# Kernel tuning notes

Hardware: AMD Instinct MI355X
Metric: run time of the kernel (lower is better)

Reference implementation:

```python
import jax, jax.numpy as jnp
import numpy as np

N_HEADS = 8
D_MODEL = 512
HEAD_DIM = D_MODEL // N_HEADS


def setup_inputs() -> dict:
    key = jax.random.key(0)
    ks = jax.random.split(key, 9)
    B, T1, T2, D = 1, 4096, 4096, D_MODEL
    w_scale = 0.02
    return {
        "query": jax.random.normal(ks[0], (B, T1, D), dtype=jnp.float32),
        "key": jax.random.normal(ks[1], (B, T2, D), dtype=jnp.float32),
        "value": jax.random.normal(ks[2], (B, T2, D), dtype=jnp.float32),
        # True = padded (masked out); ~half positions masked
        "key_padding_mask": jax.random.randint(ks[3], (B, T2), 0, 2) == 1,
        "Wq_w": jax.random.normal(ks[4], (D, D), dtype=jnp.float32) * w_scale,
        "Wq_b": jnp.zeros((D,), dtype=jnp.float32),
        "Wk_w": jax.random.normal(ks[5], (D, D), dtype=jnp.float32) * w_scale,
        "Wk_b": jnp.zeros((D,), dtype=jnp.float32),
        "Wv_w": jax.random.normal(ks[6], (D, D), dtype=jnp.float32) * w_scale,
        "Wv_b": jnp.zeros((D,), dtype=jnp.float32),
        "Wo_w": jax.random.normal(ks[7], (D, D), dtype=jnp.float32) * w_scale,
        "Wo_b": jnp.zeros((D,), dtype=jnp.float32),
    }


def reference(query, key, value, key_padding_mask,
              Wq_w, Wq_b, Wk_w, Wk_b, Wv_w, Wv_b, Wo_w, Wo_b):
    B, T1, D = query.shape
    T2 = key.shape[1]
    H, HD = N_HEADS, HEAD_DIM

    # torch Linear: y = x @ W.T + b
    q = (query @ Wq_w.T + Wq_b).reshape(B, T1, H, HD).transpose(0, 2, 1, 3)  # [B,H,T1,HD]
    k = (key @ Wk_w.T + Wk_b).reshape(B, T2, H, HD).transpose(0, 2, 1, 3)    # [B,H,T2,HD]
    v = (value @ Wv_w.T + Wv_b).reshape(B, T2, H, HD).transpose(0, 2, 1, 3)  # [B,H,T2,HD]

    scale = 1.0 / (HD ** 0.5)
    scores = jnp.einsum("bhqd,bhkd->bhqk", q, k) * scale                     # [B,H,T1,T2]
    mask_value = jnp.finfo(scores.dtype).min
    scores = jnp.where(key_padding_mask[:, None, None, :], mask_value, scores)

    attn = jax.nn.softmax(scores, axis=-1)                                   # [B,H,T1,T2]
    # dropout p=0.0 (inference) -> identity

    out = jnp.einsum("bhqk,bhkd->bhqd", attn, v)                             # [B,H,T1,HD]
    out = out.transpose(0, 2, 1, 3).reshape(B, T1, D)
    out = out @ Wo_w.T + Wo_b
    return (out, attn)
```

## Files before the change

kernel.cpp:

```cpp
#include <hip/hip_runtime.h>
#include <hip/hip_bf16.h>
#include <float.h>
#include <stdint.h>

typedef __bf16 bf16x8 __attribute__((ext_vector_type(8)));
typedef __bf16 bf16x4 __attribute__((ext_vector_type(4)));
typedef float  f32x4  __attribute__((ext_vector_type(4)));

#define T_SEQ 4096
#define DMODEL 512
#define NH 8
#define HDIM 64
#define KS1 4
#define L2E 1.44269504088896340736f

__device__ __forceinline__ float fexp2(float x) { return __builtin_amdgcn_exp2f(x); }

__device__ __forceinline__ void gl_lds16(const __bf16* g, char* l) {
    __builtin_amdgcn_global_load_lds(
        (const __attribute__((address_space(1))) unsigned int*)(g),
        (__attribute__((address_space(3))) unsigned int*)(l),
        16, 0, 0);
}

__global__ __launch_bounds__(256) void qkv_kernel(
    const float* __restrict__ qin, const float* __restrict__ kin, const float* __restrict__ vin,
    const float* __restrict__ Wq, const float* __restrict__ bq,
    const float* __restrict__ Wk, const float* __restrict__ bk,
    const float* __restrict__ Wv, const float* __restrict__ bv,
    __bf16* __restrict__ qo, __bf16* __restrict__ ko, __bf16* __restrict__ vt)
{
    __shared__ char lds[16384];
    char* Ab = lds;
    char* Bb = lds + 8192;

    const int z = blockIdx.z;
    const float* X    = (z == 0) ? qin : (z == 1) ? kin : vin;
    const float* W    = (z == 0) ? Wq  : (z == 1) ? Wk  : Wv;
    const float* bias = (z == 0) ? bq  : (z == 1) ? bk  : bv;

    const int m0 = blockIdx.x * 64;
    const int n0 = blockIdx.y * 64;
    const int tid  = threadIdx.x;
    const int w    = tid >> 6;
    const int lane = tid & 63;
    const int lrow = lane & 15;
    const int lgrp = lane >> 4;

    f32x4 acc[4] = {};
    const int r  = tid >> 2;
    const int c0 = (tid & 3) * 16;

    for (int kt = 0; kt < 8; ++kt) {
        const int k0 = kt * 64;
        const float* gA = X + (size_t)(m0 + r) * DMODEL + k0 + c0;
        const float* gB = W + (size_t)(n0 + r) * DMODEL + k0 + c0;
        const int sw = (r & 7) << 4;
#pragma unroll
        for (int i = 0; i < 4; ++i) {
            float4 a4 = *(const float4*)(gA + 4 * i);
            float4 b4 = *(const float4*)(gB + 4 * i);
            bf16x4 av, bv4;
            av[0] = (__bf16)a4.x; av[1] = (__bf16)a4.y; av[2] = (__bf16)a4.z; av[3] = (__bf16)a4.w;
            bv4[0] = (__bf16)b4.x; bv4[1] = (__bf16)b4.y; bv4[2] = (__bf16)b4.z; bv4[3] = (__bf16)b4.w;
            *(bf16x4*)(Ab + r * 128 + ((c0 * 2 + 8 * i) ^ sw)) = av;
            *(bf16x4*)(Bb + r * 128 + ((c0 * 2 + 8 * i) ^ sw)) = bv4;
        }
        __syncthreads();
#pragma unroll
        for (int ks = 0; ks < 2; ++ks) {
            bf16x8 af = *(const bf16x8*)(Ab + (w * 16 + lrow) * 128 +
                                         ((ks * 64 + lgrp * 16) ^ ((lrow & 7) << 4)));
#pragma unroll
            for (int ns = 0; ns < 4; ++ns) {
                bf16x8 bf = *(const bf16x8*)(Bb + (ns * 16 + lrow) * 128 +
                                             ((ks * 64 + lgrp * 16) ^ ((lrow & 7) << 4)));
                acc[ns] = __builtin_amdgcn_mfma_f32_16x16x32_bf16(af, bf, acc[ns], 0, 0, 0);
            }
        }
        __syncthreads();
    }

    if (z == 2) {
        char* LT = lds;
#pragma unroll
        for (int ns = 0; ns < 4; ++ns) {
            float bcol = bias[n0 + ns * 16 + lrow];
#pragma unroll
            for (int rr = 0; rr < 4; ++rr) {
                int col = ns * 16 + lrow;
                int row = w * 16 + lgrp * 4 + rr;
                *(__bf16*)(LT + col * 128 + ((row * 2) ^ ((col & 7) << 4))) =
                    (__bf16)(acc[ns][rr] + bcol);
            }
        }
        __syncthreads();
        int d  = tid >> 2;
        int nb = (tid & 3) * 32;
        bf16x8 t0 = *(const bf16x8*)(LT + d * 128 + (nb ^ ((d & 7) << 4)));
        bf16x8 t1 = *(const bf16x8*)(LT + d * 128 + ((nb + 16) ^ ((d & 7) << 4)));
        __bf16* dst = vt + (size_t)(n0 + d) * T_SEQ + m0 + (tid & 3) * 16;
        *(bf16x8*)dst = t0;
        *(bf16x8*)(dst + 8) = t1;
    } else {
        __bf16* out = (z == 0) ? qo : ko;
        const float sc = (z == 0) ? 0.125f : 1.0f;
#pragma unroll
        for (int ns = 0; ns < 4; ++ns) {
            float bcol = bias[n0 + ns * 16 + lrow];
#pragma unroll
            for (int rr = 0; rr < 4; ++rr) {
                int orow = m0 + w * 16 + lgrp * 4 + rr;
                out[(size_t)orow * DMODEL + n0 + ns * 16 + lrow] =
                    (__bf16)((acc[ns][rr] + bcol) * sc);
            }
        }
    }
}

__global__ __launch_bounds__(256) void attn_stats(
    const __bf16* __restrict__ qb, const __bf16* __restrict__ kb,
    const int* __restrict__ mask, float* __restrict__ l_part)
{
    __shared__ char lds[16384];
    char* KB0 = lds;
    char* KB1 = lds + 8192;

    const int b    = blockIdx.x;
    const int rmap = (b & 7) * ((64 * NH * KS1) / 8) + (b >> 3);
    const int qbi  = rmap & 63;
    const int h    = (rmap >> 6) & (NH - 1);
    const int ksp  = rmap >> 9;
    const int q0   = qbi * 64;
    const int k0   = ksp * (T_SEQ / KS1);

    const int tid  = threadIdx.x;
    const int w    = tid >> 6;
    const int lane = tid & 63;
    const int lrow = lane & 15;
    const int lgrp = lane >> 4;
    const int swl  = (lrow & 7) << 4;

    bf16x8 qa[2];
    {
        const __bf16* qp = qb + (size_t)(q0 + w * 16 + lrow) * DMODEL + h * HDIM;
        qa[0] = *(const bf16x8*)(qp + lgrp * 8);
        qa[1] = *(const bf16x8*)(qp + 32 + lgrp * 8);
    }

    const int key0 = w * 16 + (lane >> 3);
    const int key1 = key0 + 8;
    const int g    = lane & 7;
    const __bf16* sK0 = kb + (size_t)(k0 + key0) * DMODEL + h * HDIM + (g ^ (key0 & 7)) * 8;
    const __bf16* sK1 = kb + (size_t)(k0 + key1) * DMODEL + h * HDIM + (g ^ (key1 & 7)) * 8;

    float lsum[4] = {0.f, 0.f, 0.f, 0.f};

    gl_lds16(sK0, KB0 + w * 2048);
    gl_lds16(sK1, KB0 + w * 2048 + 1024);
    __syncthreads();

    char* cur = KB0;
    char* nxt = KB1;
    const int NT = (T_SEQ / KS1) / 64;
    for (int kt = 0; kt < NT; ++kt) {
        if (kt + 1 < NT) {
            gl_lds16(sK0 + (size_t)(kt + 1) * 64 * DMODEL, nxt + w * 2048);
            gl_lds16(sK1 + (size_t)(kt + 1) * 64 * DMODEL, nxt + w * 2048 + 1024);
        }
        float bias[4][4];
#pragma unroll
        for (int ns = 0; ns < 4; ++ns) {
            int4 mi = *(const int4*)(mask + k0 + kt * 64 + ns * 16 + lgrp * 4);
            bias[ns][0] = mi.x ? -1e30f : 0.f;
            bias[ns][1] = mi.y ? -1e30f : 0.f;
            bias[ns][2] = mi.z ? -1e30f : 0.f;
            bias[ns][3] = mi.w ? -1e30f : 0.f;
        }

        f32x4 acc[4] = {};
        __builtin_amdgcn_s_setprio(1);
#pragma unroll
        for (int ns = 0; ns < 4; ++ns) {
            bf16x8 kf0 = *(const bf16x8*)(cur + (ns * 16 + lrow) * 128 + ((lgrp * 16) ^ swl));
            bf16x8 kf1 = *(const bf16x8*)(cur + (ns * 16 + lrow) * 128 + ((64 + lgrp * 16) ^ swl));
            acc[ns] = __builtin_amdgcn_mfma_f32_16x16x32_bf16(kf0, qa[0], acc[ns], 0, 0, 0);
            acc[ns] = __builtin_amdgcn_mfma_f32_16x16x32_bf16(kf1, qa[1], acc[ns], 0, 0, 0);
        }
        __builtin_amdgcn_s_setprio(0);
#pragma unroll
        for (int ns = 0; ns < 4; ++ns)
#pragma unroll
            for (int rr = 0; rr < 4; ++rr)
                lsum[ns] += fexp2(fmaf(acc[ns][rr], L2E, bias[ns][rr]));
        __syncthreads();
        char* t = cur; cur = nxt; nxt = t;
    }

    float tot = (lsum[0] + lsum[1]) + (lsum[2] + lsum[3]);
    tot += __shfl_xor(tot, 16);
    tot += __shfl_xor(tot, 32);
    if (lgrp == 0)
        l_part[((size_t)h * KS1 + ksp) * T_SEQ + q0 + w * 16 + lrow] = tot;
}

__global__ __launch_bounds__(256) void attn_main(
    const __bf16* __restrict__ qb, const __bf16* __restrict__ kb,
    const __bf16* __restrict__ vt, const int* __restrict__ mask,
    const float* __restrict__ l_part,
    float* __restrict__ attn_out, void* __restrict__ opart,
    int KSP2, int of32)
{
    __shared__ char lds[40960];
    char* KB0 = lds;
    char* KB1 = lds + 8192;
    char* VB0 = lds + 16384;
    char* VB1 = lds + 24576;
    char* PB  = lds + 32768;

    const int nwg  = 64 * NH * KSP2;
    const int b    = blockIdx.x;
    const int rmap = (b & 7) * (nwg >> 3) + (b >> 3);
    const int qbi  = rmap & 63;
    const int h    = (rmap >> 6) & (NH - 1);
    const int kz   = rmap >> 9;
    const int q0   = qbi * 64;
    const int kspan = T_SEQ / KSP2;
    const int k0   = kz * kspan;
    const int NT   = kspan / 64;

    const int tid  = threadIdx.x;
    const int w    = tid >> 6;
    const int lane = tid & 63;
    const int lrow = lane & 15;
    const int lgrp = lane >> 4;
    const int swl  = (lrow & 7) << 4;

    bf16x8 qa[2];
    {
        const __bf16* qp = qb + (size_t)(q0 + w * 16 + lrow) * DMODEL + h * HDIM;
        qa[0] = *(const bf16x8*)(qp + lgrp * 8);
        qa[1] = *(const bf16x8*)(qp + 32 + lgrp * 8);
    }

    float rl;
    {
        float s = 0.f;
#pragma unroll
        for (int ks = 0; ks < KS1; ++ks)
            s += l_part[((size_t)h * KS1 + ks) * T_SEQ + q0 + w * 16 + lrow];
        rl = 1.0f / s;
    }

    const int key0 = w * 16 + (lane >> 3);
    const int key1 = key0 + 8;
    const int g    = lane & 7;
    const __bf16* sK0 = kb + (size_t)(k0 + key0) * DMODEL + h * HDIM + (g ^ (key0 & 7)) * 8;
    const __bf16* sK1 = kb + (size_t)(k0 + key1) * DMODEL + h * HDIM + (g ^ (key1 & 7)) * 8;
    const __bf16* sV0 = vt + (size_t)(h * HDIM + key0) * T_SEQ + k0 + (g ^ (key0 & 7)) * 8;
    const __bf16* sV1 = vt + (size_t)(h * HDIM + key1) * T_SEQ + k0 + (g ^ (key1 & 7)) * 8;

    f32x4 oacc[4] = {};
    float* arow = attn_out + (size_t)h * T_SEQ * T_SEQ +
                  (size_t)(q0 + w * 16 + lrow) * T_SEQ + k0 + lgrp * 4;
    char* Pw = PB + w * 2048;

    gl_lds16(sK0, KB0 + w * 2048);
    gl_lds16(sK1, KB0 + w * 2048 + 1024);
    gl_lds16(sV0, VB0 + w * 2048);
    gl_lds16(sV1, VB0 + w * 2048 + 1024);
    __syncthreads();

    char *kc = KB0, *kn = KB1, *vc = VB0, *vn = VB1;
    for (int kt = 0; kt < NT; ++kt) {
        if (kt + 1 < NT) {
            gl_lds16(sK0 + (size_t)(kt + 1) * 64 * DMODEL, kn + w * 2048);
            gl_lds16(sK1 + (size_t)(kt + 1) * 64 * DMODEL, kn + w * 2048 + 1024);
            gl_lds16(sV0 + (size_t)(kt + 1) * 64,          vn + w * 2048);
            gl_lds16(sV1 + (size_t)(kt + 1) * 64,          vn + w * 2048 + 1024);
        }
        float bias[4][4];
#pragma unroll
        for (int ns = 0; ns < 4; ++ns) {
            int4 mi = *(const int4*)(mask + k0 + kt * 64 + ns * 16 + lgrp * 4);
            bias[ns][0] = mi.x ? -1e30f : 0.f;
            bias[ns][1] = mi.y ? -1e30f : 0.f;
            bias[ns][2] = mi.z ? -1e30f : 0.f;
            bias[ns][3] = mi.w ? -1e30f : 0.f;
        }

        f32x4 acc[4] = {};
        __builtin_amdgcn_s_setprio(1);
#pragma unroll
        for (int ns = 0; ns < 4; ++ns) {
            bf16x8 kf0 = *(const bf16x8*)(kc + (ns * 16 + lrow) * 128 + ((lgrp * 16) ^ swl));
            bf16x8 kf1 = *(const bf16x8*)(kc + (ns * 16 + lrow) * 128 + ((64 + lgrp * 16) ^ swl));
            acc[ns] = __builtin_amdgcn_mfma_f32_16x16x32_bf16(kf0, qa[0], acc[ns], 0, 0, 0);
            acc[ns] = __builtin_amdgcn_mfma_f32_16x16x32_bf16(kf1, qa[1], acc[ns], 0, 0, 0);
        }
        __builtin_amdgcn_s_setprio(0);

        f32x4 pvs[4];
#pragma unroll
        for (int ns = 0; ns < 4; ++ns) {
            f32x4 pv;
#pragma unroll
            for (int rr = 0; rr < 4; ++rr)
                pv[rr] = fexp2(fmaf(acc[ns][rr], L2E, bias[ns][rr])) * rl;
            pvs[ns] = pv;
            bf16x4 pb;
            pb[0] = (__bf16)pv[0]; pb[1] = (__bf16)pv[1];
            pb[2] = (__bf16)pv[2]; pb[3] = (__bf16)pv[3];
            *(bf16x4*)(Pw + lrow * 128 + ((ns * 32 + lgrp * 8) ^ swl)) = pb;
        }

        __builtin_amdgcn_s_setprio(1);
#pragma unroll
        for (int ks = 0; ks < 2; ++ks) {
            bf16x8 pa = *(const bf16x8*)(Pw + lrow * 128 + ((ks * 64 + lgrp * 16) ^ swl));
#pragma unroll
            for (int dsb = 0; dsb < 4; ++dsb) {
                bf16x8 vf = *(const bf16x8*)(vc + (dsb * 16 + lrow) * 128 +
                                             ((ks * 64 + lgrp * 16) ^ swl));
                oacc[dsb] = __builtin_amdgcn_mfma_f32_16x16x32_bf16(vf, pa, oacc[dsb], 0, 0, 0);
            }
        }
        __builtin_amdgcn_s_setprio(0);

#pragma unroll
        for (int ns = 0; ns < 4; ++ns)
            *(f32x4*)(arow + kt * 64 + ns * 16) = pvs[ns];

        __syncthreads();
        char* t;
        t = kc; kc = kn; kn = t;
        t = vc; vc = vn; vn = t;
    }

    if (of32) {
        float* op = (float*)opart + (size_t)kz * T_SEQ * DMODEL +
                    (size_t)(q0 + w * 16 + lrow) * DMODEL + h * HDIM + lgrp * 4;
#pragma unroll
        for (int dsb = 0; dsb < 4; ++dsb)
            *(f32x4*)(op + dsb * 16) = oacc[dsb];
    } else {
        __bf16* op = (__bf16*)opart + (size_t)(q0 + w * 16 + lrow) * DMODEL + h * HDIM + lgrp * 4;
#pragma unroll
        for (int dsb = 0; dsb < 4; ++dsb) {
            bf16x4 ob;
            ob[0] = (__bf16)oacc[dsb][0]; ob[1] = (__bf16)oacc[dsb][1];
            ob[2] = (__bf16)oacc[dsb][2]; ob[3] = (__bf16)oacc[dsb][3];
            *(bf16x4*)(op + dsb * 16) = ob;
        }
    }
}

__global__ __launch_bounds__(256) void oproj_kernel(
    const void* __restrict__ opart, const float* __restrict__ Wo,
    const float* __restrict__ bo, float* __restrict__ out, int KSP2, int of32)
{
    __shared__ char lds[16384];
    char* Ab = lds;
    char* Bb = lds + 8192;

    const int m0 = blockIdx.x * 64;
    const int n0 = blockIdx.y * 64;
    const int tid  = threadIdx.x;
    const int w    = tid >> 6;
    const int lane = tid & 63;
    const int lrow = lane & 15;
    const int lgrp = lane >> 4;

    f32x4 acc[4] = {};
    const int r   = tid >> 2;
    const int c0e = (tid & 3) * 16;
    const int sw  = (r & 7) << 4;

    for (int kt = 0; kt < 8; ++kt) {
        const int k0 = kt * 64;
        if (of32) {
            const float* p0 = (const float*)opart + (size_t)(m0 + r) * DMODEL + k0 + c0e;
#pragma unroll
            for (int i = 0; i < 4; ++i) {
                f32x4 a4 = *(const f32x4*)(p0 + 4 * i);
                for (int s = 1; s < KSP2; ++s)
                    a4 = a4 + *(const f32x4*)(p0 + (size_t)s * T_SEQ * DMODEL + 4 * i);
                bf16x4 av;
                av[0] = (__bf16)a4[0]; av[1] = (__bf16)a4[1];
                av[2] = (__bf16)a4[2]; av[3] = (__bf16)a4[3];
                *(bf16x4*)(Ab + r * 128 + ((c0e * 2 + 8 * i) ^ sw)) = av;
            }
        } else {
            const __bf16* pa = (const __bf16*)opart + (size_t)(m0 + r) * DMODEL + k0 + c0e;
            bf16x8 a0 = *(const bf16x8*)pa;
            bf16x8 a1 = *(const bf16x8*)(pa + 8);
            *(bf16x8*)(Ab + r * 128 + ((c0e * 2) ^ sw)) = a0;
            *(bf16x8*)(Ab + r * 128 + ((c0e * 2 + 16) ^ sw)) = a1;
        }
        const float* gB = Wo + (size_t)(n0 + r) * DMODEL + k0 + c0e;
#pragma unroll
        for (int i = 0; i < 4; ++i) {
            float4 b4 = *(const float4*)(gB + 4 * i);
            bf16x4 bv4;
            bv4[0] = (__bf16)b4.x; bv4[1] = (__bf16)b4.y;
            bv4[2] = (__bf16)b4.z; bv4[3] = (__bf16)b4.w;
            *(bf16x4*)(Bb + r * 128 + ((c0e * 2 + 8 * i) ^ sw)) = bv4;
        }
        __syncthreads();
#pragma unroll
        for (int ks = 0; ks < 2; ++ks) {
            bf16x8 af = *(const bf16x8*)(Ab + (w * 16 + lrow) * 128 +
                                         ((ks * 64 + lgrp * 16) ^ ((lrow & 7) << 4)));
#pragma unroll
            for (int ns = 0; ns < 4; ++ns) {
                bf16x8 bf = *(const bf16x8*)(Bb + (ns * 16 + lrow) * 128 +
                                             ((ks * 64 + lgrp * 16) ^ ((lrow & 7) << 4)));
                acc[ns] = __builtin_amdgcn_mfma_f32_16x16x32_bf16(af, bf, acc[ns], 0, 0, 0);
            }
        }
        __syncthreads();
    }

#pragma unroll
    for (int ns = 0; ns < 4; ++ns) {
        float bcol = bo[n0 + ns * 16 + lrow];
#pragma unroll
        for (int rr = 0; rr < 4; ++rr) {
            int orow = m0 + w * 16 + lgrp * 4 + rr;
            out[(size_t)orow * DMODEL + n0 + ns * 16 + lrow] = acc[ns][rr] + bcol;
        }
    }
}

extern "C" void kernel_launch(void* const* d_in, const int* in_sizes, int n_in,
                              void* d_out, int out_size, void* d_ws, size_t ws_size,
                              hipStream_t stream) {
    const float* query = (const float*)d_in[0];
    const float* key   = (const float*)d_in[1];
    const float* value = (const float*)d_in[2];
    const int*   mask  = (const int*)d_in[3];
    const float* Wq = (const float*)d_in[4];
    const float* bq = (const float*)d_in[5];
    const float* Wk = (const float*)d_in[6];
    const float* bk = (const float*)d_in[7];
    const float* Wv = (const float*)d_in[8];
    const float* bv = (const float*)d_in[9];
    const float* Wo = (const float*)d_in[10];
    const float* bo = (const float*)d_in[11];

    float* out  = (float*)d_out;
    float* attn = out + (size_t)T_SEQ * DMODEL;

    char* ws = (char*)d_ws;
    __bf16* qo     = (__bf16*)(ws);
    __bf16* ko     = (__bf16*)(ws + (4u << 20));
    __bf16* vt     = (__bf16*)(ws + (8u << 20));
    float*  l_part = (float*)(ws + (12u << 20));
    void*   opart  = (void*)(ws + (12u << 20) + (1u << 19));
    const size_t obase = (12u << 20) + (1u << 19);

    int KSP2, of32;
    const size_t oslice = (size_t)T_SEQ * DMODEL * 4;
    if (ws_size >= obase + 4 * oslice)      { KSP2 = 4; of32 = 1; }
    else if (ws_size >= obase + 2 * oslice) { KSP2 = 2; of32 = 1; }
    else if (ws_size >= obase + oslice)     { KSP2 = 1; of32 = 1; }
    else                                    { KSP2 = 1; of32 = 0; }

    qkv_kernel<<<dim3(64, 8, 3), 256, 0, stream>>>(query, key, value,
                                                   Wq, bq, Wk, bk, Wv, bv, qo, ko, vt);
    attn_stats<<<dim3(64 * NH * KS1), 256, 0, stream>>>(qo, ko, mask, l_part);
    attn_main<<<dim3(64 * NH * KSP2), 256, 0, stream>>>(qo, ko, vt, mask, l_part,
                                                        attn, opart, KSP2, of32);
    oproj_kernel<<<dim3(64, 8), 256, 0, stream>>>(opart, Wo, bo, out, KSP2, of32);
}
```

Before: 256.2 us.

## Triple-buffer K/V tiles with explicit vmcnt waits and stage mask bias in LDS

Replaces the double-buffered K/V LDS pipeline with a three-stage ring, prefetching two tiles ahead and replacing the per-iteration __syncthreads with a partial s_waitcnt vmcnt plus s_barrier, so attention-probability stores need not drain before the next tile. The key-padding mask for the block's key span is converted once into an LDS bias array instead of being re-read from global memory every tile. Attention-probability stores are interleaved with the exp computation rather than batched after the PV MFMAs. LDS use grows to 60 KB per block, which may lower occupancy, and the hand-tuned vmcnt counts depend on the exact number of outstanding global ops.

After: 268.2 us. +4.7%, slower.

```diff
diff --git a/kernel.cpp b/kernel.cpp
--- a/kernel.cpp
+++ b/kernel.cpp
@@ -211,12 +211,9 @@
     float* __restrict__ attn_out, void* __restrict__ opart,
     int KSP2, int of32)
 {
-    __shared__ char lds[40960];
-    char* KB0 = lds;
-    char* KB1 = lds + 8192;
-    char* VB0 = lds + 16384;
-    char* VB1 = lds + 24576;
-    char* PB  = lds + 32768;
+    __shared__ char lds[61440];
+    char* PB = lds + 49152;
+    char* MB = lds + 57344;
 
     const int nwg  = 64 * NH * KSP2;
     const int b    = blockIdx.x;
@@ -252,6 +249,16 @@
         rl = 1.0f / s;
     }
 
+    {
+        int4 mi = *(const int4*)(mask + k0 + tid * 4);
+        f32x4 mb;
+        mb[0] = mi.x ? -1e30f : 0.f;
+        mb[1] = mi.y ? -1e30f : 0.f;
+        mb[2] = mi.z ? -1e30f : 0.f;
+        mb[3] = mi.w ? -1e30f : 0.f;
+        *(f32x4*)(MB + tid * 16) = mb;
+    }
+
     const int key0 = w * 16 + (lane >> 3);
     const int key1 = key0 + 8;
     const int g    = lane & 7;
@@ -260,58 +267,55 @@
     const __bf16* sV0 = vt + (size_t)(h * HDIM + key0) * T_SEQ + k0 + (g ^ (key0 & 7)) * 8;
     const __bf16* sV1 = vt + (size_t)(h * HDIM + key1) * T_SEQ + k0 + (g ^ (key1 & 7)) * 8;
 
+#define STAGE(tt, buf) do {                                             \
+        size_t koff_ = (size_t)(tt) * 64 * DMODEL;                      \
+        size_t voff_ = (size_t)(tt) * 64;                               \
+        gl_lds16(sK0 + koff_, (buf) + w * 2048);                        \
+        gl_lds16(sK1 + koff_, (buf) + w * 2048 + 1024);                 \
+        gl_lds16(sV0 + voff_, (buf) + 8192 + w * 2048);                 \
+        gl_lds16(sV1 + voff_, (buf) + 8192 + w * 2048 + 1024);          \
+    } while (0)
+
     f32x4 oacc[4] = {};
     float* arow = attn_out + (size_t)h * T_SEQ * T_SEQ +
                   (size_t)(q0 + w * 16 + lrow) * T_SEQ + k0 + lgrp * 4;
     char* Pw = PB + w * 2048;
 
-    gl_lds16(sK0, KB0 + w * 2048);
-    gl_lds16(sK1, KB0 + w * 2048 + 1024);
-    gl_lds16(sV0, VB0 + w * 2048);
-    gl_lds16(sV1, VB0 + w * 2048 + 1024);
+    char* bA = lds;
+    char* bB = lds + 16384;
+    char* bC = lds + 32768;
+
+    STAGE(0, bA);
+    STAGE(1, bB);
     __syncthreads();
 
-    char *kc = KB0, *kn = KB1, *vc = VB0, *vn = VB1;
     for (int kt = 0; kt < NT; ++kt) {
-        if (kt + 1 < NT) {
-            gl_lds16(sK0 + (size_t)(kt + 1) * 64 * DMODEL, kn + w * 2048);
-            gl_lds16(sK1 + (size_t)(kt + 1) * 64 * DMODEL, kn + w * 2048 + 1024);
-            gl_lds16(sV0 + (size_t)(kt + 1) * 64,          vn + w * 2048);
-            gl_lds16(sV1 + (size_t)(kt + 1) * 64,          vn + w * 2048 + 1024);
-        }
-        float bias[4][4];
-#pragma unroll
-        for (int ns = 0; ns < 4; ++ns) {
-            int4 mi = *(const int4*)(mask + k0 + kt * 64 + ns * 16 + lgrp * 4);
-            bias[ns][0] = mi.x ? -1e30f : 0.f;
-            bias[ns][1] = mi.y ? -1e30f : 0.f;
-            bias[ns][2] = mi.z ? -1e30f : 0.f;
-            bias[ns][3] = mi.w ? -1e30f : 0.f;
-        }
+        if (kt + 2 < NT) STAGE(kt + 2, bC);
+        __builtin_amdgcn_sched_barrier(0);
 
         f32x4 acc[4] = {};
         __builtin_amdgcn_s_setprio(1);
 #pragma unroll
         for (int ns = 0; ns < 4; ++ns) {
-            bf16x8 kf0 = *(const bf16x8*)(kc + (ns * 16 + lrow) * 128 + ((lgrp * 16) ^ swl));
-            bf16x8 kf1 = *(const bf16x8*)(kc + (ns * 16 + lrow) * 128 + ((64 + lgrp * 16) ^ swl));
+            bf16x8 kf0 = *(const bf16x8*)(bA + (ns * 16 + lrow) * 128 + ((lgrp * 16) ^ swl));
+            bf16x8 kf1 = *(const bf16x8*)(bA + (ns * 16 + lrow) * 128 + ((64 + lgrp * 16) ^ swl));
             acc[ns] = __builtin_amdgcn_mfma_f32_16x16x32_bf16(kf0, qa[0], acc[ns], 0, 0, 0);
             acc[ns] = __builtin_amdgcn_mfma_f32_16x16x32_bf16(kf1, qa[1], acc[ns], 0, 0, 0);
         }
         __builtin_amdgcn_s_setprio(0);
 
-        f32x4 pvs[4];
-#pragma unroll
-        for (int ns = 0; ns < 4; ++ns) {
+#pragma unroll
+        for (int ns = 0; ns < 4; ++ns) {
+            f32x4 mb = *(const f32x4*)(MB + ((kt * 64 + ns * 16 + lgrp * 4) << 2));
             f32x4 pv;
 #pragma unroll
             for (int rr = 0; rr < 4; ++rr)
-                pv[rr] = fexp2(fmaf(acc[ns][rr], L2E, bias[ns][rr])) * rl;
-            pvs[ns] = pv;
+                pv[rr] = fexp2(fmaf(acc[ns][rr], L2E, mb[rr])) * rl;
             bf16x4 pb;
             pb[0] = (__bf16)pv[0]; pb[1] = (__bf16)pv[1];
             pb[2] = (__bf16)pv[2]; pb[3] = (__bf16)pv[3];
             *(bf16x4*)(Pw + lrow * 128 + ((ns * 32 + lgrp * 8) ^ swl)) = pb;
+            *(f32x4*)(arow + kt * 64 + ns * 16) = pv;
         }
 
         __builtin_amdgcn_s_setprio(1);
@@ -320,22 +324,22 @@
             bf16x8 pa = *(const bf16x8*)(Pw + lrow * 128 + ((ks * 64 + lgrp * 16) ^ swl));
 #pragma unroll
             for (int dsb = 0; dsb < 4; ++dsb) {
-                bf16x8 vf = *(const bf16x8*)(vc + (dsb * 16 + lrow) * 128 +
+                bf16x8 vf = *(const bf16x8*)(bA + 8192 + (dsb * 16 + lrow) * 128 +
                                              ((ks * 64 + lgrp * 16) ^ swl));
                 oacc[dsb] = __builtin_amdgcn_mfma_f32_16x16x32_bf16(vf, pa, oacc[dsb], 0, 0, 0);
             }
         }
         __builtin_amdgcn_s_setprio(0);
 
-#pragma unroll
-        for (int ns = 0; ns < 4; ++ns)
-            *(f32x4*)(arow + kt * 64 + ns * 16) = pvs[ns];
-
-        __syncthreads();
-        char* t;
-        t = kc; kc = kn; kn = t;
-        t = vc; vc = vn; vn = t;
-    }
+        if (kt + 1 < NT) {
+            if (kt == NT - 2) asm volatile("s_waitcnt vmcnt(8)" ::: "memory");
+            else              asm volatile("s_waitcnt vmcnt(12)" ::: "memory");
+            __builtin_amdgcn_s_barrier();
+            __builtin_amdgcn_sched_barrier(0);
+        }
+        char* tmp = bA; bA = bB; bB = bC; bC = tmp;
+    }
+#undef STAGE
 
     if (of32) {
         float* op = (float*)opart + (size_t)kz * T_SEQ * DMODEL +
```
